# Performance work log

Measured on AMD Instinct MI355X. Metric: run time of the kernel, lower is better.

Reference implementation:

```python
import jax, jax.numpy as jnp
import numpy as np

NUM_HEADS = 4
LN_EPS = 1e-5
L2_EPS = 1e-12


def setup_inputs() -> dict:
    key = jax.random.key(0)
    ks = jax.random.split(key, 10)
    B, L, D, Hd = 256, 197, 768, 512
    dh = Hd // NUM_HEADS  # 128
    NC = 1000
    sc = lambda k, shape, s: jax.random.normal(k, shape, jnp.float32) * s
    return {
        "cls_token": jax.random.normal(ks[0], (B, D), jnp.float32),
        "x": jax.random.normal(ks[1], (B, L, D), jnp.float32),
        "proj_w": sc(ks[2], (D, Hd), 0.02),
        "proj_b": jnp.zeros((Hd,), jnp.float32),
        "ln_g": jnp.ones((dh,), jnp.float32),
        "ln_b": jnp.zeros((dh,), jnp.float32),
        "conv1_w": sc(ks[3], (3, 3, 3, 3), 0.2),
        "conv2_w": sc(ks[4], (3, 3, 3, 3), 0.2),
        "cls1_w": sc(ks[5], (D, NC), 0.02),
        "cls1_b": jnp.zeros((NC,), jnp.float32),
        "cls2_w": sc(ks[6], (2883, NC), 0.02),
        "cls2_b": jnp.zeros((NC,), jnp.float32),
    }


def reference(cls_token, x, proj_w, proj_b, ln_g, ln_b, conv1_w, conv2_w,
              cls1_w, cls1_b, cls2_w, cls2_b):
    B, L, D = x.shape
    dh = ln_g.shape[0]
    # proj on patch tokens (drop cls at position 0)
    xp = x[:, 1:, :] @ proj_w + proj_b            # (B, 196, 512)
    Lp = xp.shape[1]
    H = xp.shape[2] // dh
    heads = xp.reshape(B, Lp, H, dh).transpose(2, 0, 1, 3)  # (H, B, Lp, dh)
    # LayerNorm over last dim (eps=1e-5, biased var, affine)
    mu = heads.mean(-1, keepdims=True)
    var = heads.var(-1, keepdims=True)
    hn = (heads - mu) * jax.lax.rsqrt(var + LN_EPS) * ln_g + ln_b
    # Covariance._remove_mean: adaptive_avg_pool2d on (B, dh, Lp) -> mean over BOTH dh and Lp per sample
    hn = hn - hn.mean(axis=(2, 3), keepdims=True)
    # 'near' cross-covariances between adjacent heads, all pairs batched
    x1, x2 = hn[:-1], hn[1:]                      # (H-1, B, Lp, dh)
    cov = jnp.einsum('pbnd,pbne->pbde', x1, x2) / Lp  # (H-1, B, dh, dh)
    # L2 normalize over dim=2 (row axis of each dh x dh map), F.normalize eps
    nrm = jnp.sqrt(jnp.sum(cov * cov, axis=2, keepdims=True))
    cov = cov / jnp.maximum(nrm, L2_EPS)
    cov = cov.transpose(1, 0, 2, 3)               # (B, 3, 128, 128)
    conv = lambda z, w: jax.lax.conv_general_dilated(
        z, w, (2, 2), 'VALID', dimension_numbers=('NCHW', 'OIHW', 'NCHW'))
    z = conv(cov, conv1_w)                        # (B, 3, 63, 63)
    z = jax.nn.gelu(z, approximate=False)
    z = conv(z, conv2_w)                          # (B, 3, 31, 31)
    flat = z.reshape(B, -1)                       # (B, 2883)
    out = ((cls_token @ cls1_w + cls1_b) + (flat @ cls2_w + cls2_b)) / 2
    return out
```

## Files before the change

### kernel.cpp

```cpp
#include <hip/hip_runtime.h>
#include <hip/hip_bf16.h>
#include <cstdint>

typedef __bf16 bf16_t;
typedef __bf16 bf16x4 __attribute__((ext_vector_type(4)));
typedef __bf16 bf16x8 __attribute__((ext_vector_type(8)));
typedef float floatx4 __attribute__((ext_vector_type(4)));
typedef unsigned int u32;
typedef unsigned short ushort8 __attribute__((ext_vector_type(8)));
typedef unsigned int u32x2 __attribute__((ext_vector_type(2)));

#define LNEPS 1e-5f

__device__ inline void async_copy16(const bf16_t* g, bf16_t* l) {
    __builtin_amdgcn_global_load_lds((const __attribute__((address_space(1))) void*)g,
                                     (__attribute__((address_space(3))) void*)l,
                                     16, 0, 0);
}

__global__ __launch_bounds__(256)
void k_cvt_x(const float* __restrict__ x, bf16_t* __restrict__ xbf) {
    const int vid = blockIdx.x * 256 + threadIdx.x;
    const int row = vid / 96;
    const int kv  = vid - row * 96;
    const int b = row / 196, l = row - (row / 196) * 196;
    const float* src = x + ((b * 197 + l + 1) * 96 + kv) * 8;
    const floatx4 f0 = *(const floatx4*)src;
    const floatx4 f1 = *(const floatx4*)(src + 4);
    bf16x8 o;
#pragma unroll
    for (int e = 0; e < 4; e++) { o[e] = (bf16_t)f0[e]; o[e+4] = (bf16_t)f1[e]; }
    *(bf16x8*)(xbf + vid * 8) = o;
}

__global__ __launch_bounds__(256)
void k_transpose_w(const float* __restrict__ w, bf16_t* __restrict__ wt) {
    __shared__ bf16_t tile[32][33];
    const int bx = blockIdx.x;
    const int by = blockIdx.y;
    const int tx = threadIdx.x & 31, ty = threadIdx.x >> 5;
    for (int i = ty; i < 32; i += 8)
        tile[i][tx] = (bf16_t)w[(by*32 + i)*512 + bx*32 + tx];
    __syncthreads();
    for (int i = ty; i < 32; i += 8)
        wt[(bx*32 + i)*768 + by*32 + tx] = tile[tx][i];
}

__global__ __launch_bounds__(256, 3)
void k_proj_ln(const bf16_t* __restrict__ xbf, const bf16_t* __restrict__ wt,
               const float* __restrict__ pb, const float* __restrict__ lng,
               const float* __restrict__ lnb, bf16_t* __restrict__ hn,
               float* __restrict__ csum)
{
    __shared__ bf16_t As[3][128*32];
    __shared__ bf16_t Bs[3][128*32];

    const int t = threadIdx.x;
    const int lane = t & 63;
    const int wv = t >> 6;
    const int q = lane >> 4;
    const int c = lane & 15;
    const int L = blockIdx.x;
    const int xcd = L & 7, slot = L >> 3;
    const int h = slot & 3;
    const int m0 = (xcd + 8 * (slot >> 2)) * 128;

    const int srow  = t >> 2;
    const int skoff = (t & 3) * 8;
    const bf16_t* ag = xbf + (m0 + srow) * 768 + skoff;
    const bf16_t* bg = wt + (h*128 + srow) * 768 + skoff;

#define STAGE(B, kk)                                                     \
    {                                                                    \
        const int kn_ = (kk) * 32;                                       \
        async_copy16(ag + kn_,          &As[B][t*8]);                    \
        async_copy16(ag + 64*768 + kn_, &As[B][2048 + t*8]);             \
        async_copy16(bg + kn_,          &Bs[B][t*8]);                    \
        async_copy16(bg + 64*768 + kn_, &Bs[B][2048 + t*8]);             \
    }

#define COMPUTE(B)                                                       \
    {                                                                    \
        bf16x8 af[2], bfr[8];                                            \
        _Pragma("unroll")                                                \
        for (int i = 0; i < 2; i++)                                      \
            af[i] = *(const bf16x8*)&As[B][(wv*32 + i*16 + c)*32 + q*8]; \
        _Pragma("unroll")                                                \
        for (int j = 0; j < 8; j++)                                      \
            bfr[j] = *(const bf16x8*)&Bs[B][(j*16 + c)*32 + q*8];        \
        _Pragma("unroll")                                                \
        for (int i = 0; i < 2; i++)                                      \
            _Pragma("unroll")                                            \
            for (int j = 0; j < 8; j++)                                  \
                acc[i][j] = __builtin_amdgcn_mfma_f32_16x16x32_bf16(af[i], bfr[j], acc[i][j], 0, 0, 0); \
    }

    floatx4 acc[2][8];
#pragma unroll
    for (int i = 0; i < 2; i++)
#pragma unroll
        for (int j = 0; j < 8; j++)
#pragma unroll
            for (int r = 0; r < 4; r++) acc[i][j][r] = 0.f;

    STAGE(0, 0);
    STAGE(1, 1);
    STAGE(2, 2);

    for (int ks = 0; ks < 22; ks++) {
        const int buf = ks % 3;
        asm volatile("s_waitcnt vmcnt(8)" ::: "memory");
        __builtin_amdgcn_s_barrier();
        COMPUTE(buf);
        __builtin_amdgcn_s_barrier();
        if (ks < 21) STAGE(buf, ks + 3);
    }
    asm volatile("s_waitcnt vmcnt(4)" ::: "memory");
    __builtin_amdgcn_s_barrier();
    COMPUTE(1);
    __builtin_amdgcn_s_barrier();
    asm volatile("s_waitcnt vmcnt(0)" ::: "memory");
    __builtin_amdgcn_s_barrier();
    COMPUTE(2);

#undef STAGE
#undef COMPUTE

    float bias[8], gg[8], bb[8];
#pragma unroll
    for (int j = 0; j < 8; j++) {
        const int d = j*16 + c;
        bias[j] = pb[h*128 + d];
        gg[j]   = lng[d];
        bb[j]   = lnb[d];
    }
    float cs0[8], cs1[8];
#pragma unroll
    for (int j = 0; j < 8; j++) { cs0[j] = 0.f; cs1[j] = 0.f; }
    const int b0 = m0 / 196;
    const int bL = (m0 + 127) / 196;
#pragma unroll
    for (int i = 0; i < 2; i++) {
#pragma unroll
        for (int r = 0; r < 4; r++) {
            float s = 0.f, s2 = 0.f;
#pragma unroll
            for (int j = 0; j < 8; j++) {
                const float v = acc[i][j][r] + bias[j];
                acc[i][j][r] = v;
                s += v; s2 += v*v;
            }
#pragma unroll
            for (int o = 1; o < 16; o <<= 1) { s += __shfl_xor(s, o); s2 += __shfl_xor(s2, o); }
            const float mu = s * (1.f/128.f);
            const float ms = s2 * (1.f/128.f);
            const float rstd = rsqrtf(ms - mu*mu + LNEPS);
            const int gm = m0 + wv*32 + i*16 + q*4 + r;
            const int bI = gm / 196, l = gm - bI*196;
            bf16_t* dst = hn + (((h*256 + bI)*196 + l) << 7);
            const bool first = (bI == b0);
#pragma unroll
            for (int j = 0; j < 8; j++) {
                const float v = (acc[i][j][r] - mu)*rstd*gg[j] + bb[j];
                dst[j*16 + c] = (bf16_t)v;
                cs0[j] += first ? v : 0.f;
                cs1[j] += first ? 0.f : v;
            }
        }
    }
    float* scr = (float*)As;
#pragma unroll
    for (int j = 0; j < 8; j++) {
        float s0 = cs0[j], s1 = cs1[j];
        s0 += __shfl_xor(s0, 16); s0 += __shfl_xor(s0, 32);
        s1 += __shfl_xor(s1, 16); s1 += __shfl_xor(s1, 32);
        if (q == 0) {
            scr[(wv*2 + 0)*128 + j*16 + c] = s0;
            scr[(wv*2 + 1)*128 + j*16 + c] = s1;
        }
    }
    __syncthreads();
    {
        const int bucket = t >> 7, d = t & 127;
        if (bucket == 0 || bL > b0) {
            const float s = scr[(0*2 + bucket)*128 + d] + scr[(1*2 + bucket)*128 + d]
                          + scr[(2*2 + bucket)*128 + d] + scr[(3*2 + bucket)*128 + d];
            atomicAdd(&csum[((h*256 + b0 + bucket) << 7) + d], s);
        }
    }
}

__global__ __launch_bounds__(256, 3)
void k_cov(const bf16_t* __restrict__ hn, const float* __restrict__ colsum,
           float* __restrict__ cov)
{
    __shared__ u32 x1s[128*18];
    __shared__ u32 x2s[128*18];
    __shared__ float rs1[128], rs2[128];
    __shared__ float colsq[2][128];
    __shared__ float nrm_inv[128];
    __shared__ float mu_s[2];

    const int t = threadIdx.x;
    const int lane = t & 63;
    const int wv = t >> 6;
    const int wr = wv >> 1, wc = wv & 1;
    const int q = lane >> 4;
    const int c = lane & 15;
    const int b = blockIdx.x;
    const int p = blockIdx.y;

    const bf16_t* X1 = hn + (((p*256 + b)*196) << 7);
    const bf16_t* X2 = hn + ((((p+1)*256 + b)*196) << 7);

    if (t < 128) rs1[t] = colsum[((p*256 + b) << 7) + t];
    else         rs2[t & 127] = colsum[(((p+1)*256 + b) << 7) + (t & 127)];
    __syncthreads();
    if (wv == 0) {
        float s = rs1[lane] + rs1[lane + 64];
#pragma unroll
        for (int o = 1; o < 64; o <<= 1) s += __shfl_xor(s, o);
        if (lane == 0) mu_s[0] = s * (1.f/(196.f*128.f));
    } else if (wv == 1) {
        float s = rs2[lane] + rs2[lane + 64];
#pragma unroll
        for (int o = 1; o < 64; o <<= 1) s += __shfl_xor(s, o);
        if (lane == 0) mu_s[1] = s * (1.f/(196.f*128.f));
    }

    floatx4 acc[4][4];
#pragma unroll
    for (int i = 0; i < 4; i++)
#pragma unroll
        for (int j = 0; j < 4; j++)
#pragma unroll
            for (int r = 0; r < 4; r++) acc[i][j][r] = 0.f;

    const int np  = t & 15;
    const int dch = t >> 4;

    ushort8 cva, cvb, cwa, cwb;
    {
        const int na = 2*np, nb = na + 1;
        cva = *(const ushort8*)(X1 + (na << 7) + dch*8);
        cwa = *(const ushort8*)(X2 + (na << 7) + dch*8);
        cvb = *(const ushort8*)(X1 + (nb << 7) + dch*8);
        cwb = *(const ushort8*)(X2 + (nb << 7) + dch*8);
    }

    for (int n0 = 0; n0 < 224; n0 += 32) {
        __syncthreads();
#pragma unroll
        for (int e = 0; e < 8; e++) {
            x1s[(dch*8 + e)*18 + np] = (u32)cva[e] | ((u32)cvb[e] << 16);
            x2s[(dch*8 + e)*18 + np] = (u32)cwa[e] | ((u32)cwb[e] << 16);
        }
        __syncthreads();
        if (n0 + 32 < 224) {
            const int na = n0 + 32 + 2*np, nb = na + 1;
            ushort8 z;
#pragma unroll
            for (int e = 0; e < 8; e++) z[e] = 0;
            ushort8 nva = z, nvb = z, nwa = z, nwb = z;
            if (na < 196) {
                nva = *(const ushort8*)(X1 + (na << 7) + dch*8);
                nwa = *(const ushort8*)(X2 + (na << 7) + dch*8);
            }
            if (nb < 196) {
                nvb = *(const ushort8*)(X1 + (nb << 7) + dch*8);
                nwb = *(const ushort8*)(X2 + (nb << 7) + dch*8);
            }
            cva = nva; cvb = nvb; cwa = nwa; cwb = nwb;
        }
        bf16x8 af[4], bfr[4];
#pragma unroll
        for (int i = 0; i < 4; i++) {
            const int base = (wr*64 + i*16 + c)*18 + q*4;
            u32 tmp[4];
            *(u32x2*)&tmp[0] = *(const u32x2*)&x1s[base];
            *(u32x2*)&tmp[2] = *(const u32x2*)&x1s[base + 2];
            __builtin_memcpy(&af[i], tmp, 16);
        }
#pragma unroll
        for (int j = 0; j < 4; j++) {
            const int base = (wc*64 + j*16 + c)*18 + q*4;
            u32 tmp[4];
            *(u32x2*)&tmp[0] = *(const u32x2*)&x2s[base];
            *(u32x2*)&tmp[2] = *(const u32x2*)&x2s[base + 2];
            __builtin_memcpy(&bfr[j], tmp, 16);
        }
#pragma unroll
        for (int i = 0; i < 4; i++)
#pragma unroll
            for (int j = 0; j < 4; j++)
                acc[i][j] = __builtin_amdgcn_mfma_f32_16x16x32_bf16(af[i], bfr[j], acc[i][j], 0, 0, 0);
    }

    const float mu1 = mu_s[0], mu2 = mu_s[1];
    const float invL = 1.f/196.f;
    float csq[4] = {0.f, 0.f, 0.f, 0.f};
#pragma unroll
    for (int i = 0; i < 4; i++)
#pragma unroll
        for (int j = 0; j < 4; j++)
#pragma unroll
            for (int r = 0; r < 4; r++) {
                const int d = wr*64 + i*16 + q*4 + r;
                const int e = wc*64 + j*16 + c;
                const float v = acc[i][j][r]*invL - mu2*rs1[d]*invL - mu1*rs2[e]*invL + mu1*mu2;
                acc[i][j][r] = v;
                csq[j] += v*v;
            }
#pragma unroll
    for (int j = 0; j < 4; j++) {
        float s = csq[j];
        s += __shfl_xor(s, 16);
        s += __shfl_xor(s, 32);
        csq[j] = s;
    }
    if (q == 0) {
#pragma unroll
        for (int j = 0; j < 4; j++) colsq[wr][wc*64 + j*16 + c] = csq[j];
    }
    __syncthreads();
    if (t < 128) {
        const float nr = sqrtf(colsq[0][t] + colsq[1][t]);
        nrm_inv[t] = 1.f / fmaxf(nr, 1e-12f);
    }
    __syncthreads();
    float* dst = cov + ((long)b*3 + p)*16384;
#pragma unroll
    for (int i = 0; i < 4; i++)
#pragma unroll
        for (int j = 0; j < 4; j++) {
            const int e = wc*64 + j*16 + c;
            const float ni = nrm_inv[e];
#pragma unroll
            for (int r = 0; r < 4; r++) {
                const int d = wr*64 + i*16 + q*4 + r;
                dst[(d << 7) + e] = acc[i][j][r] * ni;
            }
        }
}

__global__ __launch_bounds__(256)
void k_convs(const float* __restrict__ cov, const float* __restrict__ w1,
             const float* __restrict__ w2, bf16_t* __restrict__ Xb)
{
    __shared__ float Z[3*33*63];
    __shared__ float W1s[81];
    __shared__ float W2s[81];
    const int t = threadIdx.x;
    const int b = blockIdx.x >> 1, half = blockIdx.x & 1;
    const int zy0 = half ? 32 : 0;
    const int nzy = half ? 31 : 33;
    const int y20 = half ? 16 : 0;
    const int ny2 = half ? 15 : 16;
    if (t < 81) { W1s[t] = w1[t]; W2s[t] = w2[t]; }
    __syncthreads();
    const float* C = cov + (long)b*3*16384;
    const int ztot = 3*nzy*63;
    for (int idx = t; idx < ztot; idx += 256) {
        const int o = idx / (nzy*63), rem = idx - o*(nzy*63);
        const int yl = rem / 63, xx = rem - yl*63;
        const int y = zy0 + yl;
        float a = 0.f;
#pragma unroll
        for (int i = 0; i < 3; i++) {
            const float* Ci = C + i*16384 + (2*y)*128 + 2*xx;
            const float* Wi = &W1s[o*27 + i*9];
            a += Ci[0]*Wi[0]   + Ci[1]*Wi[1]   + Ci[2]*Wi[2]
               + Ci[128]*Wi[3] + Ci[129]*Wi[4] + Ci[130]*Wi[5]
               + Ci[256]*Wi[6] + Ci[257]*Wi[7] + Ci[258]*Wi[8];
        }
        Z[o*2079 + yl*63 + xx] = 0.5f*a*(1.0f + erff(a*0.70710678118654752f));
    }
    __syncthreads();
    const int c2tot = 3*ny2*31;
    for (int idx = t; idx < c2tot; idx += 256) {
        const int o = idx / (ny2*31), rem = idx - o*(ny2*31);
        const int y2l = rem / 31, x2 = rem - y2l*31;
        float a = 0.f;
#pragma unroll
        for (int i = 0; i < 3; i++) {
            const float* Zi = Z + i*2079 + (2*y2l)*63 + 2*x2;
            const float* Wi = &W2s[(o*3+i)*9];
            a += Zi[0]*Wi[0]   + Zi[1]*Wi[1]   + Zi[2]*Wi[2]
               + Zi[63]*Wi[3]  + Zi[64]*Wi[4]  + Zi[65]*Wi[5]
               + Zi[126]*Wi[6] + Zi[127]*Wi[7] + Zi[128]*Wi[8];
        }
        const int oy2 = y20 + y2l;
        Xb[(long)b*3712 + 768 + o*961 + oy2*31 + x2] = (bf16_t)a;
    }
}

__global__ __launch_bounds__(256)
void k_cvt_cls(const float* __restrict__ cls, bf16_t* __restrict__ Xb,
               float* __restrict__ csum)
{
    const int t = threadIdx.x, b = blockIdx.x;
    for (int k = t; k < 768; k += 256)
        Xb[b*3712 + k] = (bf16_t)cls[b*768 + k];
    if (t < 61) Xb[b*3712 + 3651 + t] = (bf16_t)0.f;
    float* cz = csum + b*512;
    cz[t] = 0.f; cz[t + 256] = 0.f;
}

__global__ __launch_bounds__(256)
void k_cvt_w(const float* __restrict__ W1, const float* __restrict__ W2,
             bf16_t* __restrict__ Wb)
{
    __shared__ bf16_t tile[32][33];
    const int k0 = blockIdx.x * 32;
    const int n0 = blockIdx.y * 32;
    const int tx = threadIdx.x & 31, ty = threadIdx.x >> 5;
    for (int i = ty; i < 32; i += 8) {
        const int k = k0 + i, n = n0 + tx;
        float v = 0.f;
        if (n < 1000 && k < 3651)
            v = (k < 768) ? W1[k*1000 + n] : W2[(k-768)*1000 + n];
        tile[i][tx] = (bf16_t)v;
    }
    __syncthreads();
    for (int i = ty; i < 32; i += 8)
        Wb[(n0 + i)*3712 + k0 + tx] = tile[tx][i];
}

__global__ __launch_bounds__(256, 2)
void k_gemm_cls(const bf16_t* __restrict__ Xb, const bf16_t* __restrict__ Wb,
                float* __restrict__ partial)
{
    __shared__ bf16_t As[3][128*32];
    __shared__ bf16_t Bs[3][128*32];

    const int t = threadIdx.x;
    const int lane = t & 63;
    const int wv = t >> 6;
    const int wr = wv >> 1, wc = wv & 1;
    const int q = lane >> 4;
    const int c = lane & 15;
    const int nt = blockIdx.x;
    const int mt = blockIdx.y;
    const int sp = blockIdx.z;

    const int srow  = t >> 2;
    const int skoff = (t & 3) * 8;
    const int m0 = mt * 128, n0 = nt * 128;
    const int kbase = sp * 928;
    const bf16_t* ag0 = Xb + (m0 + srow) * 3712 + kbase + skoff;
    const bf16_t* ag1 = Xb + (m0 + srow + 64) * 3712 + kbase + skoff;
    const bf16_t* bg0 = Wb + (n0 + srow) * 3712 + kbase + skoff;
    const bf16_t* bg1 = Wb + (n0 + srow + 64) * 3712 + kbase + skoff;

#define GSTAGE(B, kk)                                                    \
    {                                                                    \
        const int kn_ = (kk) * 32;                                       \
        async_copy16(ag0 + kn_, &As[B][t*8]);                            \
        async_copy16(ag1 + kn_, &As[B][2048 + t*8]);                     \
        async_copy16(bg0 + kn_, &Bs[B][t*8]);                            \
        async_copy16(bg1 + kn_, &Bs[B][2048 + t*8]);                     \
    }

#define GCOMPUTE(B)                                                      \
    {                                                                    \
        bf16x8 af[4], bfr[4];                                            \
        _Pragma("unroll")                                                \
        for (int i = 0; i < 4; i++)                                      \
            af[i] = *(const bf16x8*)&As[B][(wr*64 + i*16 + c)*32 + q*8]; \
        _Pragma("unroll")                                                \
        for (int j = 0; j < 4; j++)                                      \
            bfr[j] = *(const bf16x8*)&Bs[B][(wc*64 + j*16 + c)*32 + q*8];\
        _Pragma("unroll")                                                \
        for (int i = 0; i < 4; i++)                                      \
            _Pragma("unroll")                                            \
            for (int j = 0; j < 4; j++)                                  \
                acc[i][j] = __builtin_amdgcn_mfma_f32_16x16x32_bf16(af[i], bfr[j], acc[i][j], 0, 0, 0); \
    }

    floatx4 acc[4][4];
#pragma unroll
    for (int i = 0; i < 4; i++)
#pragma unroll
        for (int j = 0; j < 4; j++)
#pragma unroll
            for (int r = 0; r < 4; r++) acc[i][j][r] = 0.f;

    GSTAGE(0, 0);
    GSTAGE(1, 1);
    GSTAGE(2, 2);

    for (int ks = 0; ks < 27; ks++) {
        const int buf = ks % 3;
        asm volatile("s_waitcnt vmcnt(8)" ::: "memory");
        __builtin_amdgcn_s_barrier();
        GCOMPUTE(buf);
        __builtin_amdgcn_s_barrier();
        if (ks < 26) GSTAGE(buf, ks + 3);
    }
    asm volatile("s_waitcnt vmcnt(4)" ::: "memory");
    __builtin_amdgcn_s_barrier();
    GCOMPUTE(0);
    __builtin_amdgcn_s_barrier();
    asm volatile("s_waitcnt vmcnt(0)" ::: "memory");
    __builtin_amdgcn_s_barrier();
    GCOMPUTE(1);

#undef GSTAGE
#undef GCOMPUTE

    float* base = partial + ((long)sp*256 + m0)*1024 + n0;
#pragma unroll
    for (int i = 0; i < 4; i++)
#pragma unroll
        for (int r = 0; r < 4; r++) {
            const int row = wr*64 + i*16 + q*4 + r;
#pragma unroll
            for (int j = 0; j < 4; j++)
                base[row*1024 + wc*64 + j*16 + c] = acc[i][j][r];
        }
}

__global__ __launch_bounds__(256)
void k_cls_fin(const float* __restrict__ partial, const float* __restrict__ b1,
               const float* __restrict__ b2, float* __restrict__ out)
{
    const int idx = blockIdx.x * 256 + threadIdx.x;
    const int m = idx / 1000, n = idx - m*1000;
    float s = partial[(m)*1024 + n] + partial[(256 + m)*1024 + n]
            + partial[(512 + m)*1024 + n] + partial[(768 + m)*1024 + n];
    out[idx] = 0.5f*(s + b1[n] + b2[n]);
}

extern "C" void kernel_launch(void* const* d_in, const int* in_sizes, int n_in,
                              void* d_out, int out_size, void* d_ws, size_t ws_size,
                              hipStream_t stream) {
    const float* cls = (const float*)d_in[0];
    const float* x   = (const float*)d_in[1];
    const float* pw  = (const float*)d_in[2];
    const float* pb  = (const float*)d_in[3];
    const float* lng = (const float*)d_in[4];
    const float* lnb = (const float*)d_in[5];
    const float* c1w = (const float*)d_in[6];
    const float* c2w = (const float*)d_in[7];
    const float* w1  = (const float*)d_in[8];
    const float* b1  = (const float*)d_in[9];
    const float* w2  = (const float*)d_in[10];
    const float* b2  = (const float*)d_in[11];

    char* ws = (char*)d_ws;
    bf16_t* hn    = (bf16_t*)(ws);
    bf16_t* xbf   = (bf16_t*)(ws + 51380224ull);
    float*  covb  = (float*) (ws + 51380224ull);
    bf16_t* wt    = (bf16_t*)(ws + 128450560ull);
    float*  csum  = (float*) (ws + 129236992ull);
    bf16_t* Xb    = (bf16_t*)(ws + 129761280ull);
    bf16_t* Wb    = (bf16_t*)(ws + 131661824ull);
    float*  part  = (float*) (ws + 139264000ull);
    float*  out   = (float*)d_out;

    k_transpose_w<<<dim3(16, 24), 256, 0, stream>>>(pw, wt);
    k_cvt_x<<<18816, 256, 0, stream>>>(x, xbf);
    k_cvt_cls<<<256, 256, 0, stream>>>(cls, Xb, csum);
    k_cvt_w<<<dim3(116, 32), 256, 0, stream>>>(w1, w2, Wb);
    k_proj_ln<<<1568, 256, 0, stream>>>(xbf, wt, pb, lng, lnb, hn, csum);
    k_cov<<<dim3(256, 3), 256, 0, stream>>>(hn, csum, covb);
    k_convs<<<512, 256, 0, stream>>>(covb, c1w, c2w, Xb);
    k_gemm_cls<<<dim3(8, 2, 4), 256, 0, stream>>>(Xb, Wb, part);
    k_cls_fin<<<1000, 256, 0, stream>>>(part, b1, b2, out);
}
```

Baseline: 408.7 us.

## Load A operand directly to registers in proj GEMM, drop A LDS buffers

The projection GEMM kernel now loads its A-operand (activation) fragments straight from global memory into registers, using a three-set register rotation with a two-step prefetch. Only the B (weight) tiles still stage through LDS via async copies. Removing the A LDS buffers halves shared memory use and drops the LDS reads for A, which lets the launch bounds target 4 blocks per CU instead of 3. The costs are uncoalesced-ish direct global loads for A, higher register pressure from the extra fragment sets, and trickier vmcnt accounting across the unrolled pipeline.

```diff
diff --git a/kernel.cpp b/kernel.cpp
--- a/kernel.cpp
+++ b/kernel.cpp
@@ -46,13 +46,12 @@
         wt[(bx*32 + i)*768 + by*32 + tx] = tile[tx][i];
 }
 
-__global__ __launch_bounds__(256, 3)
+__global__ __launch_bounds__(256, 4)
 void k_proj_ln(const bf16_t* __restrict__ xbf, const bf16_t* __restrict__ wt,
                const float* __restrict__ pb, const float* __restrict__ lng,
                const float* __restrict__ lnb, bf16_t* __restrict__ hn,
                float* __restrict__ csum)
 {
-    __shared__ bf16_t As[3][128*32];
     __shared__ bf16_t Bs[3][128*32];
 
     const int t = threadIdx.x;
@@ -65,36 +64,36 @@
     const int h = slot & 3;
     const int m0 = (xcd + 8 * (slot >> 2)) * 128;
 
-    const int srow  = t >> 2;
-    const int skoff = (t & 3) * 8;
-    const bf16_t* ag = xbf + (m0 + srow) * 768 + skoff;
-    const bf16_t* bg = wt + (h*128 + srow) * 768 + skoff;
-
-#define STAGE(B, kk)                                                     \
+    const bf16_t* aP0 = xbf + (size_t)(m0 + wv*32 + c) * 768 + q*8;
+    const bf16_t* aP1 = aP0 + 16*768;
+    const bf16_t* bg = wt + (h*128 + (t >> 2)) * 768 + (t & 3) * 8;
+
+#define BSTG(B, kk)                                                      \
     {                                                                    \
-        const int kn_ = (kk) * 32;                                       \
-        async_copy16(ag + kn_,          &As[B][t*8]);                    \
-        async_copy16(ag + 64*768 + kn_, &As[B][2048 + t*8]);             \
-        async_copy16(bg + kn_,          &Bs[B][t*8]);                    \
-        async_copy16(bg + 64*768 + kn_, &Bs[B][2048 + t*8]);             \
-    }
-
-#define COMPUTE(B)                                                       \
+        async_copy16(bg + (kk)*32,          &Bs[B][t*8]);                \
+        async_copy16(bg + 64*768 + (kk)*32, &Bs[B][2048 + t*8]);         \
+    }
+#define ALD(SET, kk)                                                     \
     {                                                                    \
-        bf16x8 af[2], bfr[8];                                            \
+        SET[0] = *(const bf16x8*)(aP0 + (kk)*32);                        \
+        SET[1] = *(const bf16x8*)(aP1 + (kk)*32);                        \
+    }
+#define PSTEP(BUF, AC, AN, WN, DA, DB, ks)                               \
+    {                                                                    \
+        asm volatile("s_waitcnt vmcnt(" #WN ")" ::: "memory");           \
+        __builtin_amdgcn_s_barrier();                                    \
         _Pragma("unroll")                                                \
-        for (int i = 0; i < 2; i++)                                      \
-            af[i] = *(const bf16x8*)&As[B][(wv*32 + i*16 + c)*32 + q*8]; \
-        _Pragma("unroll")                                                \
-        for (int j = 0; j < 8; j++)                                      \
-            bfr[j] = *(const bf16x8*)&Bs[B][(j*16 + c)*32 + q*8];        \
-        _Pragma("unroll")                                                \
-        for (int i = 0; i < 2; i++)                                      \
-            _Pragma("unroll")                                            \
-            for (int j = 0; j < 8; j++)                                  \
-                acc[i][j] = __builtin_amdgcn_mfma_f32_16x16x32_bf16(af[i], bfr[j], acc[i][j], 0, 0, 0); \
-    }
-
+        for (int j_ = 0; j_ < 8; j_++) {                                 \
+            const bf16x8 bfr_ = *(const bf16x8*)&Bs[BUF][(j_*16 + c)*32 + q*8]; \
+            acc[0][j_] = __builtin_amdgcn_mfma_f32_16x16x32_bf16(AC[0], bfr_, acc[0][j_], 0, 0, 0); \
+            acc[1][j_] = __builtin_amdgcn_mfma_f32_16x16x32_bf16(AC[1], bfr_, acc[1][j_], 0, 0, 0); \
+        }                                                                \
+        __builtin_amdgcn_s_barrier();                                    \
+        if (DA) ALD(AN, (ks) + 2);                                       \
+        if (DB) BSTG(BUF, (ks) + 3);                                     \
+    }
+
+    bf16x8 a0[2], a1[2], a2[2];
     floatx4 acc[2][8];
 #pragma unroll
     for (int i = 0; i < 2; i++)
@@ -103,28 +102,29 @@
 #pragma unroll
             for (int r = 0; r < 4; r++) acc[i][j][r] = 0.f;
 
-    STAGE(0, 0);
-    STAGE(1, 1);
-    STAGE(2, 2);
-
-    for (int ks = 0; ks < 22; ks++) {
-        const int buf = ks % 3;
-        asm volatile("s_waitcnt vmcnt(8)" ::: "memory");
-        __builtin_amdgcn_s_barrier();
-        COMPUTE(buf);
-        __builtin_amdgcn_s_barrier();
-        if (ks < 21) STAGE(buf, ks + 3);
-    }
-    asm volatile("s_waitcnt vmcnt(4)" ::: "memory");
-    __builtin_amdgcn_s_barrier();
-    COMPUTE(1);
-    __builtin_amdgcn_s_barrier();
-    asm volatile("s_waitcnt vmcnt(0)" ::: "memory");
-    __builtin_amdgcn_s_barrier();
-    COMPUTE(2);
-
-#undef STAGE
-#undef COMPUTE
+    BSTG(0, 0);
+    asm volatile("" ::: "memory");
+    ALD(a0, 0);
+    asm volatile("" ::: "memory");
+    BSTG(1, 1);
+    asm volatile("" ::: "memory");
+    ALD(a1, 1);
+    asm volatile("" ::: "memory");
+    BSTG(2, 2);
+
+    for (int t3 = 0; t3 < 7; t3++) {
+        const int ks = t3 * 3;
+        PSTEP(0, a0, a2, 6, 1, 1, ks);
+        PSTEP(1, a1, a0, 6, 1, 1, ks + 1);
+        PSTEP(2, a2, a1, 6, 1, 1, ks + 2);
+    }
+    PSTEP(0, a0, a2, 6, 1, 0, 21);
+    PSTEP(1, a1, a0, 4, 0, 0, 22);
+    PSTEP(2, a2, a1, 0, 0, 0, 23);
+
+#undef BSTG
+#undef ALD
+#undef PSTEP
 
     float bias[8], gg[8], bb[8];
 #pragma unroll
@@ -168,7 +168,7 @@
             }
         }
     }
-    float* scr = (float*)As;
+    float* scr = (float*)Bs;
 #pragma unroll
     for (int j = 0; j < 8; j++) {
         float s0 = cs0[j], s1 = cs1[j];
```

After: 414.9 us. No clear change (+1.5%).
